# Kernel optimization log

Measured on AMD Instinct MI355X. Metric: run time of the kernel, lower is better.

## Reference

```python
import jax, jax.numpy as jnp
import numpy as np

D_MODEL = 1024
D_STATE = 128
SEQ_LEN = 4096
BATCH = 4
N_FFT = 2 ** int(np.ceil(np.log2(2 * SEQ_LEN - 1)))  # 8192
LN_EPS = 1e-3  # keras LayerNormalization default epsilon


def setup_inputs() -> dict:
    key = jax.random.key(0)
    ks = jax.random.split(key, 12)
    def dense_w(k, fan_in, fan_out):
        lim = np.sqrt(6.0 / (fan_in + fan_out)).astype(np.float32)  # glorot uniform
        return jax.random.uniform(k, (fan_in, fan_out), jnp.float32, -lim, lim)
    return {
        "x": jax.random.normal(ks[0], (BATCH, SEQ_LEN, D_MODEL), jnp.float32),
        "ln_gamma": jnp.ones((D_MODEL,), jnp.float32),
        "ln_beta": jnp.zeros((D_MODEL,), jnp.float32),
        "W_in": dense_w(ks[1], D_MODEL, D_MODEL),
        "b_in": jnp.zeros((D_MODEL,), jnp.float32),
        "W_xs": dense_w(ks[2], D_MODEL, D_STATE),
        "W_B": dense_w(ks[3], D_MODEL, D_STATE),
        "b_B": jnp.zeros((D_STATE,), jnp.float32),
        "W_C": dense_w(ks[4], D_MODEL, D_STATE),
        "b_C": jnp.zeros((D_STATE,), jnp.float32),
        "A_log": jax.random.uniform(ks[5], (D_STATE,), jnp.float32, -4.0, -1.0),
        "D": jnp.ones((D_MODEL,), jnp.float32),
        "W_so": dense_w(ks[6], D_STATE, D_MODEL),
        "W_out": dense_w(ks[7], D_MODEL, D_MODEL),
        "b_out": jnp.zeros((D_MODEL,), jnp.float32),
    }


def reference(x, ln_gamma, ln_beta, W_in, b_in, W_xs, W_B, b_B, W_C, b_C,
              A_log, D, W_so, W_out, b_out):
    residual = x
    # LayerNorm over last dim
    mu = jnp.mean(x, axis=-1, keepdims=True)
    var = jnp.mean(jnp.square(x - mu), axis=-1, keepdims=True)
    xn = (x - mu) * jax.lax.rsqrt(var + LN_EPS) * ln_gamma + ln_beta
    # projections
    z = xn @ W_in + b_in                      # [B, L, d_model]
    x_state = z @ W_xs                        # [B, L, d_state]
    B_sel = z @ W_B + b_B                     # [B, L, d_state]
    C_sel = z @ W_C + b_C                     # [B, L, d_state]
    # stable A-parameterization -> kernel K[t, s] = exp(A_s * t)
    A = -jnp.exp(A_log)                       # [d_state]
    t = jnp.arange(SEQ_LEN, dtype=jnp.float32)
    K = jnp.exp(t[:, None] * A[None, :])      # [L, d_state]
    # FFT convolution along time axis (zero-padded to N_FFT, causal slice)
    u = x_state * B_sel                       # [B, L, d_state]
    u_f = jnp.fft.rfft(u, n=N_FFT, axis=1)    # [B, N_FFT//2+1, d_state]
    k_f = jnp.fft.rfft(K, n=N_FFT, axis=0)    # [N_FFT//2+1, d_state]
    y_state = jnp.fft.irfft(u_f * k_f[None], n=N_FFT, axis=1)[:, :SEQ_LEN]
    y_state = y_state * C_sel
    # output path with skip connection through D
    y = y_state @ W_so + D * z                # [B, L, d_model]
    y = y @ W_out + b_out
    return y + residual
```

## Files before the change

kernel.cpp:

```cpp
#include <hip/hip_runtime.h>
#include <math.h>

#define D_MODEL 1024
#define D_STATE 128
#define SEQ_LEN 4096
#define BATCH 4
#define NTOK (BATCH * SEQ_LEN)
#define LN_EPS 1e-3f
#define NCHUNK 64
#define LCHUNK (SEQ_LEN / NCHUNK)

typedef __attribute__((ext_vector_type(8))) short bf16x8;
typedef __attribute__((ext_vector_type(4))) float f32x4;

__device__ __forceinline__ short f2bf(float f) {
    union { float f; unsigned u; } v; v.f = f;
    unsigned r = v.u + 0x7FFFu + ((v.u >> 16) & 1u);
    return (short)(r >> 16);
}
__device__ __forceinline__ float bf2f(short s) {
    union { unsigned u; float f; } v; v.u = ((unsigned)(unsigned short)s) << 16;
    return v.f;
}

__global__ __launch_bounds__(256) void ln_kernel(const float* __restrict__ x,
                                                 const float* __restrict__ gamma,
                                                 const float* __restrict__ beta,
                                                 short* __restrict__ xn_bf) {
    int row = blockIdx.x;
    const float4* xr = (const float4*)(x + (size_t)row * D_MODEL);
    float4 v = xr[threadIdx.x];
    float s1 = v.x + v.y + v.z + v.w;
    float s2 = v.x * v.x + v.y * v.y + v.z * v.z + v.w * v.w;
    for (int off = 32; off; off >>= 1) {
        s1 += __shfl_down(s1, off);
        s2 += __shfl_down(s2, off);
    }
    __shared__ float ls1[4], ls2[4];
    int wid = threadIdx.x >> 6, lane = threadIdx.x & 63;
    if (lane == 0) { ls1[wid] = s1; ls2[wid] = s2; }
    __syncthreads();
    s1 = ls1[0] + ls1[1] + ls1[2] + ls1[3];
    s2 = ls2[0] + ls2[1] + ls2[2] + ls2[3];
    float mu = s1 * (1.0f / D_MODEL);
    float var = s2 * (1.0f / D_MODEL) - mu * mu;
    float r = rsqrtf(var + LN_EPS);
    float4 g = ((const float4*)gamma)[threadIdx.x];
    float4 b = ((const float4*)beta)[threadIdx.x];
    short4 o;
    o.x = f2bf((v.x - mu) * r * g.x + b.x);
    o.y = f2bf((v.y - mu) * r * g.y + b.y);
    o.z = f2bf((v.z - mu) * r * g.z + b.z);
    o.w = f2bf((v.w - mu) * r * g.w + b.w);
    ((short4*)(xn_bf + (size_t)row * D_MODEL))[threadIdx.x] = o;
}

__global__ __launch_bounds__(256) void transpose_bf(const float* __restrict__ in,
                                                    short* __restrict__ out,
                                                    int K, int N) {
    __shared__ float t[32][33];
    int nb = blockIdx.x * 32, kb = blockIdx.y * 32;
    int tx = threadIdx.x, ty = threadIdx.y;
#pragma unroll
    for (int i = 0; i < 4; ++i)
        t[ty + 8 * i][tx] = in[(size_t)(kb + ty + 8 * i) * N + nb + tx];
    __syncthreads();
#pragma unroll
    for (int i = 0; i < 4; ++i)
        out[(size_t)(nb + ty + 8 * i) * K + kb + tx] = f2bf(t[tx][ty + 8 * i]);
}

__global__ void build_bias3(const float* __restrict__ bB, const float* __restrict__ bC,
                            float* __restrict__ bias3) {
    int n = blockIdx.x * 128 + threadIdx.x;
    bias3[n] = (n < 128) ? 0.f : ((n < 256) ? bB[n - 128] : bC[n - 256]);
}

template<int HAS_BIAS, int HAS_ADD, int ADD_BF, int HAS_SCALE, int OUT_F32, int OUT_BF, int SWZ>
__global__ __launch_bounds__(256) void gemm_bf16(
    const short* __restrict__ A, const short* __restrict__ BT,
    const float* __restrict__ bias,
    const float* __restrict__ addf, const short* __restrict__ addb,
    const float* __restrict__ addscale,
    float* __restrict__ Cf, short* __restrict__ Cbf,
    int Mt, int Nt, int K) {
    __shared__ short As[128 * 32];
    __shared__ short Bs[128 * 32];
    int p = blockIdx.x;
    int mtile, ntile;
    if (SWZ) {
        int k = p & 7, q = p >> 3;
        ntile = q & 7;
        mtile = k + 8 * (q >> 3);
    } else {
        mtile = p % Mt;
        ntile = p / Mt;
    }
    int m0 = mtile * 128, n0 = ntile * 128;
    int N = Nt * 128;
    int tid = threadIdx.x;
    int lane = tid & 63;
    int w = tid >> 6;
    int quad = lane >> 4, r16 = lane & 15;
    int wm = (w & 1) * 64, wn = (w >> 1) * 64;

    f32x4 acc[4][4] = {};

    for (int k0 = 0; k0 < K; k0 += 32) {
#pragma unroll
        for (int it = 0; it < 2; ++it) {
            int seg = it * 256 + tid;
            int row = seg >> 2, sc = seg & 3;
            const short* gp = A + (size_t)(m0 + row) * K + k0 + sc * 8;
            __builtin_amdgcn_global_load_lds(
                (const __attribute__((address_space(1))) unsigned*)gp,
                (__attribute__((address_space(3))) unsigned*)(As + seg * 8), 16, 0, 0);
        }
#pragma unroll
        for (int it = 0; it < 2; ++it) {
            int seg = it * 256 + tid;
            int row = seg >> 2, sc = seg & 3;
            const short* gp = BT + (size_t)(n0 + row) * K + k0 + sc * 8;
            __builtin_amdgcn_global_load_lds(
                (const __attribute__((address_space(1))) unsigned*)gp,
                (__attribute__((address_space(3))) unsigned*)(Bs + seg * 8), 16, 0, 0);
        }
        __syncthreads();

        const short* ap = As + (wm + r16) * 32 + quad * 8;
        const short* bp = Bs + (wn + r16) * 32 + quad * 8;
        bf16x8 af[4], bfr[4];
#pragma unroll
        for (int i = 0; i < 4; ++i) af[i] = *(const bf16x8*)(ap + i * 16 * 32);
#pragma unroll
        for (int j = 0; j < 4; ++j) bfr[j] = *(const bf16x8*)(bp + j * 16 * 32);
#pragma unroll
        for (int i = 0; i < 4; ++i)
#pragma unroll
            for (int j = 0; j < 4; ++j)
                acc[i][j] = __builtin_amdgcn_mfma_f32_16x16x32_bf16(af[i], bfr[j], acc[i][j], 0, 0, 0);
        __syncthreads();
    }

#pragma unroll
    for (int i = 0; i < 4; ++i) {
#pragma unroll
        for (int j = 0; j < 4; ++j) {
            int col = n0 + wn + j * 16 + r16;
            float bv = HAS_BIAS ? bias[col] : 0.f;
            float sc = HAS_SCALE ? addscale[col] : 1.f;
#pragma unroll
            for (int pr = 0; pr < 4; ++pr) {
                int row = m0 + wm + i * 16 + quad * 4 + pr;
                float v = acc[i][j][pr] + bv;
                if (HAS_ADD) {
                    float av = ADD_BF ? bf2f(addb[(size_t)row * N + col])
                                      : addf[(size_t)row * N + col];
                    v += sc * av;
                }
                if (OUT_F32) Cf[(size_t)row * N + col] = v;
                if (OUT_BF) Cbf[(size_t)row * N + col] = f2bf(v);
            }
        }
    }
}

__global__ __launch_bounds__(128) void scan_p1(const float* __restrict__ s3,
                                               const float* __restrict__ A_log,
                                               float* __restrict__ hbuf,
                                               float* __restrict__ Ebuf) {
    int s = threadIdx.x;
    int c = blockIdx.x, b = blockIdx.y;
    float a = expf(-expf(A_log[s]));
    float h = 0.f;
    size_t base = (size_t)b * SEQ_LEN + (size_t)c * LCHUNK;
    for (int i = 0; i < LCHUNK; ++i) {
        size_t r = base + i;
        float u = s3[r * 384 + s] * s3[r * 384 + 128 + s];
        h = a * h + u;
        hbuf[r * 128 + s] = h;
    }
    Ebuf[((size_t)b * NCHUNK + c) * 128 + s] = h;
}

__global__ __launch_bounds__(512) void scan_p2(const float* __restrict__ A_log,
                                               const float* __restrict__ Ebuf,
                                               float* __restrict__ Gbuf) {
    int tid = threadIdx.x;
    int b = tid >> 7, s = tid & 127;
    float A = -expf(A_log[s]);
    float pw = expf(A * (float)LCHUNK);
    float e[NCHUNK];
#pragma unroll
    for (int c = 0; c < NCHUNK; ++c)
        e[c] = Ebuf[((size_t)b * NCHUNK + c) * 128 + s];
    float G = 0.f;
#pragma unroll
    for (int c = 0; c < NCHUNK; ++c) {
        G = pw * G + e[c];
        Gbuf[((size_t)b * NCHUNK + c) * 128 + s] = G;
    }
}

__global__ __launch_bounds__(128) void scan_p3(const float* __restrict__ s3,
                                               const float* __restrict__ A_log,
                                               const float* __restrict__ hbuf,
                                               const float* __restrict__ Gbuf,
                                               short* __restrict__ ys_bf) {
    int s = threadIdx.x;
    int c = blockIdx.x, b = blockIdx.y;
    float a = expf(-expf(A_log[s]));
    float carry = (c == 0) ? 0.f : Gbuf[((size_t)b * NCHUNK + c - 1) * 128 + s];
    float p = a;
    size_t base = (size_t)b * SEQ_LEN + (size_t)c * LCHUNK;
    for (int i = 0; i < LCHUNK; ++i) {
        size_t r = base + i;
        float h = hbuf[r * 128 + s] + p * carry;
        p *= a;
        ys_bf[r * 128 + s] = f2bf(h * s3[r * 384 + 256 + s]);
    }
}

extern "C" void kernel_launch(void* const* d_in, const int* in_sizes, int n_in,
                              void* d_out, int out_size, void* d_ws, size_t ws_size,
                              hipStream_t stream) {
    const float* x     = (const float*)d_in[0];
    const float* ln_g  = (const float*)d_in[1];
    const float* ln_b  = (const float*)d_in[2];
    const float* W_in  = (const float*)d_in[3];
    const float* b_in  = (const float*)d_in[4];
    const float* W_xs  = (const float*)d_in[5];
    const float* W_B   = (const float*)d_in[6];
    const float* b_B   = (const float*)d_in[7];
    const float* W_C   = (const float*)d_in[8];
    const float* b_C   = (const float*)d_in[9];
    const float* A_log = (const float*)d_in[10];
    const float* Dvec  = (const float*)d_in[11];
    const float* W_so  = (const float*)d_in[12];
    const float* W_out = (const float*)d_in[13];
    const float* b_out = (const float*)d_in[14];
    float* out = (float*)d_out;

    char* w = (char*)d_ws;
    size_t off = 0;
    short* xn_bf = (short*)(w + off);
    float* hbuf  = (float*)(w + off);
    short* ys_bf = (short*)(w + off + 8388608);
    off += (size_t)NTOK * D_MODEL * 2;
    short* z_bf  = (short*)(w + off);
    off += (size_t)NTOK * D_MODEL * 2;
    short* y1_bf = (short*)(w + off);
    off += (size_t)NTOK * D_MODEL * 2;
    float* s3    = (float*)(w + off); off += (size_t)NTOK * 384 * 4;
    float* Ebuf  = (float*)(w + off); off += (size_t)BATCH * NCHUNK * 128 * 4;
    float* Gbuf  = (float*)(w + off); off += (size_t)BATCH * NCHUNK * 128 * 4;
    short* W_inT  = (short*)(w + off); off += (size_t)D_MODEL * D_MODEL * 2;
    short* W3T    = (short*)(w + off); off += (size_t)384 * D_MODEL * 2;
    short* W_soT  = (short*)(w + off); off += (size_t)D_MODEL * D_STATE * 2;
    short* W_outT = (short*)(w + off); off += (size_t)D_MODEL * D_MODEL * 2;
    float* bias3  = (float*)(w + off); off += 2048;

    dim3 tb(32, 8);
    transpose_bf<<<dim3(D_MODEL / 32, D_MODEL / 32), tb, 0, stream>>>(W_in, W_inT, D_MODEL, D_MODEL);
    transpose_bf<<<dim3(D_STATE / 32, D_MODEL / 32), tb, 0, stream>>>(W_xs, W3T, D_MODEL, D_STATE);
    transpose_bf<<<dim3(D_STATE / 32, D_MODEL / 32), tb, 0, stream>>>(W_B, W3T + 128 * D_MODEL, D_MODEL, D_STATE);
    transpose_bf<<<dim3(D_STATE / 32, D_MODEL / 32), tb, 0, stream>>>(W_C, W3T + 256 * D_MODEL, D_MODEL, D_STATE);
    transpose_bf<<<dim3(D_MODEL / 32, D_STATE / 32), tb, 0, stream>>>(W_so, W_soT, D_STATE, D_MODEL);
    transpose_bf<<<dim3(D_MODEL / 32, D_MODEL / 32), tb, 0, stream>>>(W_out, W_outT, D_MODEL, D_MODEL);
    build_bias3<<<3, 128, 0, stream>>>(b_B, b_C, bias3);

    ln_kernel<<<NTOK, 256, 0, stream>>>(x, ln_g, ln_b, xn_bf);

    const int Mt = NTOK / 128;
    gemm_bf16<1, 0, 0, 0, 0, 1, 1><<<Mt * 8, 256, 0, stream>>>(
        xn_bf, W_inT, b_in, nullptr, nullptr, nullptr,
        nullptr, z_bf, Mt, 8, D_MODEL);

    gemm_bf16<1, 0, 0, 0, 1, 0, 0><<<Mt * 3, 256, 0, stream>>>(
        z_bf, W3T, bias3, nullptr, nullptr, nullptr,
        s3, nullptr, Mt, 3, D_MODEL);

    scan_p1<<<dim3(NCHUNK, BATCH), 128, 0, stream>>>(s3, A_log, hbuf, Ebuf);
    scan_p2<<<1, 512, 0, stream>>>(A_log, Ebuf, Gbuf);
    scan_p3<<<dim3(NCHUNK, BATCH), 128, 0, stream>>>(s3, A_log, hbuf, Gbuf, ys_bf);

    gemm_bf16<0, 1, 1, 1, 0, 1, 1><<<Mt * 8, 256, 0, stream>>>(
        ys_bf, W_soT, nullptr, nullptr, z_bf, Dvec,
        nullptr, y1_bf, Mt, 8, D_STATE);

    gemm_bf16<1, 1, 0, 0, 1, 0, 1><<<Mt * 8, 256, 0, stream>>>(
        y1_bf, W_outT, b_out, x, nullptr, nullptr,
        out, nullptr, Mt, 8, D_MODEL);
}
```

Measured before the change: 338.0 us.

## Widen GEMM K-tile with XOR-swizzled LDS, fuse prep kernels, retune scan chunks

The GEMM now stages a K=64 slice per iteration using an XOR swizzle in LDS to avoid bank conflicts, and sets a launch-bounds occupancy hint. This halves the barrier count per K step. The six weight transposes and the bias build are merged into one launch to cut launch overhead. The scan uses twice as many chunks for more parallelism, with partial unrolling and a register-blocked second pass. The larger LDS footprint and the occupancy hint may limit registers or occupancy.

```diff
diff --git a/kernel.cpp b/kernel.cpp
--- a/kernel.cpp
+++ b/kernel.cpp
@@ -7,7 +7,7 @@
 #define BATCH 4
 #define NTOK (BATCH * SEQ_LEN)
 #define LN_EPS 1e-3f
-#define NCHUNK 64
+#define NCHUNK 128
 #define LCHUNK (SEQ_LEN / NCHUNK)
 
 typedef __attribute__((ext_vector_type(8))) short bf16x8;
@@ -55,37 +55,51 @@
     ((short4*)(xn_bf + (size_t)row * D_MODEL))[threadIdx.x] = o;
 }
 
-__global__ __launch_bounds__(256) void transpose_bf(const float* __restrict__ in,
-                                                    short* __restrict__ out,
-                                                    int K, int N) {
-    __shared__ float t[32][33];
-    int nb = blockIdx.x * 32, kb = blockIdx.y * 32;
+__global__ __launch_bounds__(256) void prep_kernel(
+    const float* __restrict__ W_in, const float* __restrict__ W_xs,
+    const float* __restrict__ W_B, const float* __restrict__ W_C,
+    const float* __restrict__ W_so, const float* __restrict__ W_out,
+    const float* __restrict__ bB, const float* __restrict__ bC,
+    short* __restrict__ W_inT, short* __restrict__ W3T,
+    short* __restrict__ W_soT, short* __restrict__ W_outT,
+    float* __restrict__ bias3) {
+    int blk = blockIdx.x;
+    const float* in; short* out; int K, N, tile;
+    if (blk < 1024)      { in = W_in;  out = W_inT;           K = 1024; N = 1024; tile = blk; }
+    else if (blk < 1152) { in = W_xs;  out = W3T;             K = 1024; N = 128;  tile = blk - 1024; }
+    else if (blk < 1280) { in = W_B;   out = W3T + 128*1024;  K = 1024; N = 128;  tile = blk - 1152; }
+    else if (blk < 1408) { in = W_C;   out = W3T + 256*1024;  K = 1024; N = 128;  tile = blk - 1280; }
+    else if (blk < 1536) { in = W_so;  out = W_soT;           K = 128;  N = 1024; tile = blk - 1408; }
+    else if (blk < 2560) { in = W_out; out = W_outT;          K = 1024; N = 1024; tile = blk - 1536; }
+    else {
+        int t = threadIdx.y * 32 + threadIdx.x;
+        for (int n = t; n < 384; n += 256)
+            bias3[n] = (n < 128) ? 0.f : ((n < 256) ? bB[n - 128] : bC[n - 256]);
+        return;
+    }
+    __shared__ float t32[32][33];
+    int ntiles = N / 32;
+    int nb = (tile % ntiles) * 32, kb = (tile / ntiles) * 32;
     int tx = threadIdx.x, ty = threadIdx.y;
 #pragma unroll
     for (int i = 0; i < 4; ++i)
-        t[ty + 8 * i][tx] = in[(size_t)(kb + ty + 8 * i) * N + nb + tx];
+        t32[ty + 8 * i][tx] = in[(size_t)(kb + ty + 8 * i) * N + nb + tx];
     __syncthreads();
 #pragma unroll
     for (int i = 0; i < 4; ++i)
-        out[(size_t)(nb + ty + 8 * i) * K + kb + tx] = f2bf(t[tx][ty + 8 * i]);
-}
-
-__global__ void build_bias3(const float* __restrict__ bB, const float* __restrict__ bC,
-                            float* __restrict__ bias3) {
-    int n = blockIdx.x * 128 + threadIdx.x;
-    bias3[n] = (n < 128) ? 0.f : ((n < 256) ? bB[n - 128] : bC[n - 256]);
+        out[(size_t)(nb + ty + 8 * i) * K + kb + tx] = f2bf(t32[tx][ty + 8 * i]);
 }
 
 template<int HAS_BIAS, int HAS_ADD, int ADD_BF, int HAS_SCALE, int OUT_F32, int OUT_BF, int SWZ>
-__global__ __launch_bounds__(256) void gemm_bf16(
+__global__ __launch_bounds__(256, 4) void gemm_bf16(
     const short* __restrict__ A, const short* __restrict__ BT,
     const float* __restrict__ bias,
     const float* __restrict__ addf, const short* __restrict__ addb,
     const float* __restrict__ addscale,
     float* __restrict__ Cf, short* __restrict__ Cbf,
     int Mt, int Nt, int K) {
-    __shared__ short As[128 * 32];
-    __shared__ short Bs[128 * 32];
+    __shared__ short As[128 * 64];
+    __shared__ short Bs[128 * 64];
     int p = blockIdx.x;
     int mtile, ntile;
     if (SWZ) {
@@ -106,39 +120,46 @@
 
     f32x4 acc[4][4] = {};
 
-    for (int k0 = 0; k0 < K; k0 += 32) {
-#pragma unroll
-        for (int it = 0; it < 2; ++it) {
+    for (int k0 = 0; k0 < K; k0 += 64) {
+#pragma unroll
+        for (int it = 0; it < 4; ++it) {
             int seg = it * 256 + tid;
-            int row = seg >> 2, sc = seg & 3;
-            const short* gp = A + (size_t)(m0 + row) * K + k0 + sc * 8;
+            int row = seg >> 3, slot = seg & 7;
+            int kc8 = slot ^ (row & 7);
+            const short* gp = A + (size_t)(m0 + row) * K + k0 + kc8 * 8;
             __builtin_amdgcn_global_load_lds(
                 (const __attribute__((address_space(1))) unsigned*)gp,
                 (__attribute__((address_space(3))) unsigned*)(As + seg * 8), 16, 0, 0);
         }
 #pragma unroll
-        for (int it = 0; it < 2; ++it) {
+        for (int it = 0; it < 4; ++it) {
             int seg = it * 256 + tid;
-            int row = seg >> 2, sc = seg & 3;
-            const short* gp = BT + (size_t)(n0 + row) * K + k0 + sc * 8;
+            int row = seg >> 3, slot = seg & 7;
+            int kc8 = slot ^ (row & 7);
+            const short* gp = BT + (size_t)(n0 + row) * K + k0 + kc8 * 8;
             __builtin_amdgcn_global_load_lds(
                 (const __attribute__((address_space(1))) unsigned*)gp,
                 (__attribute__((address_space(3))) unsigned*)(Bs + seg * 8), 16, 0, 0);
         }
         __syncthreads();
 
-        const short* ap = As + (wm + r16) * 32 + quad * 8;
-        const short* bp = Bs + (wn + r16) * 32 + quad * 8;
-        bf16x8 af[4], bfr[4];
-#pragma unroll
-        for (int i = 0; i < 4; ++i) af[i] = *(const bf16x8*)(ap + i * 16 * 32);
-#pragma unroll
-        for (int j = 0; j < 4; ++j) bfr[j] = *(const bf16x8*)(bp + j * 16 * 32);
-#pragma unroll
-        for (int i = 0; i < 4; ++i)
-#pragma unroll
-            for (int j = 0; j < 4; ++j)
-                acc[i][j] = __builtin_amdgcn_mfma_f32_16x16x32_bf16(af[i], bfr[j], acc[i][j], 0, 0, 0);
+        const short* abase = As + (wm + r16) * 64;
+        const short* bbase = Bs + (wn + r16) * 64;
+        int sw = r16 & 7;
+#pragma unroll
+        for (int kk = 0; kk < 2; ++kk) {
+            int phys = ((quad + 4 * kk) ^ sw) * 8;
+            bf16x8 af[4], bfr[4];
+#pragma unroll
+            for (int i = 0; i < 4; ++i) af[i] = *(const bf16x8*)(abase + i * 16 * 64 + phys);
+#pragma unroll
+            for (int j = 0; j < 4; ++j) bfr[j] = *(const bf16x8*)(bbase + j * 16 * 64 + phys);
+#pragma unroll
+            for (int i = 0; i < 4; ++i)
+#pragma unroll
+                for (int j = 0; j < 4; ++j)
+                    acc[i][j] = __builtin_amdgcn_mfma_f32_16x16x32_bf16(af[i], bfr[j], acc[i][j], 0, 0, 0);
+        }
         __syncthreads();
     }
 
@@ -174,6 +195,7 @@
     float a = expf(-expf(A_log[s]));
     float h = 0.f;
     size_t base = (size_t)b * SEQ_LEN + (size_t)c * LCHUNK;
+#pragma unroll 8
     for (int i = 0; i < LCHUNK; ++i) {
         size_t r = base + i;
         float u = s3[r * 384 + s] * s3[r * 384 + 128 + s];
@@ -188,17 +210,18 @@
                                                float* __restrict__ Gbuf) {
     int tid = threadIdx.x;
     int b = tid >> 7, s = tid & 127;
-    float A = -expf(A_log[s]);
-    float pw = expf(A * (float)LCHUNK);
-    float e[NCHUNK];
-#pragma unroll
-    for (int c = 0; c < NCHUNK; ++c)
-        e[c] = Ebuf[((size_t)b * NCHUNK + c) * 128 + s];
+    float pw = expf(-expf(A_log[s]) * (float)LCHUNK);
     float G = 0.f;
-#pragma unroll
-    for (int c = 0; c < NCHUNK; ++c) {
-        G = pw * G + e[c];
-        Gbuf[((size_t)b * NCHUNK + c) * 128 + s] = G;
+    for (int c0 = 0; c0 < NCHUNK; c0 += 16) {
+        float e[16];
+#pragma unroll
+        for (int t = 0; t < 16; ++t)
+            e[t] = Ebuf[((size_t)b * NCHUNK + c0 + t) * 128 + s];
+#pragma unroll
+        for (int t = 0; t < 16; ++t) {
+            G = pw * G + e[t];
+            Gbuf[((size_t)b * NCHUNK + c0 + t) * 128 + s] = G;
+        }
     }
 }
 
@@ -213,6 +236,7 @@
     float carry = (c == 0) ? 0.f : Gbuf[((size_t)b * NCHUNK + c - 1) * 128 + s];
     float p = a;
     size_t base = (size_t)b * SEQ_LEN + (size_t)c * LCHUNK;
+#pragma unroll 8
     for (int i = 0; i < LCHUNK; ++i) {
         size_t r = base + i;
         float h = hbuf[r * 128 + s] + p * carry;
@@ -260,14 +284,8 @@
     short* W_outT = (short*)(w + off); off += (size_t)D_MODEL * D_MODEL * 2;
     float* bias3  = (float*)(w + off); off += 2048;
 
-    dim3 tb(32, 8);
-    transpose_bf<<<dim3(D_MODEL / 32, D_MODEL / 32), tb, 0, stream>>>(W_in, W_inT, D_MODEL, D_MODEL);
-    transpose_bf<<<dim3(D_STATE / 32, D_MODEL / 32), tb, 0, stream>>>(W_xs, W3T, D_MODEL, D_STATE);
-    transpose_bf<<<dim3(D_STATE / 32, D_MODEL / 32), tb, 0, stream>>>(W_B, W3T + 128 * D_MODEL, D_MODEL, D_STATE);
-    transpose_bf<<<dim3(D_STATE / 32, D_MODEL / 32), tb, 0, stream>>>(W_C, W3T + 256 * D_MODEL, D_MODEL, D_STATE);
-    transpose_bf<<<dim3(D_MODEL / 32, D_STATE / 32), tb, 0, stream>>>(W_so, W_soT, D_STATE, D_MODEL);
-    transpose_bf<<<dim3(D_MODEL / 32, D_MODEL / 32), tb, 0, stream>>>(W_out, W_outT, D_MODEL, D_MODEL);
-    build_bias3<<<3, 128, 0, stream>>>(b_B, b_C, bias3);
+    prep_kernel<<<2561, dim3(32, 8), 0, stream>>>(W_in, W_xs, W_B, W_C, W_so, W_out,
+                                                  b_B, b_C, W_inT, W3T, W_soT, W_outT, bias3);
 
     ln_kernel<<<NTOK, 256, 0, stream>>>(x, ln_g, ln_b, xn_bf);
 
```

New measurement: 284.2 us. 15.9% less time.
